# Kernel optimization log

Hardware: AMD Instinct MI355X
Metric: run time of the kernel (lower is better)

Reference implementation:

```python
import jax, jax.numpy as jnp
import numpy as np

B, T, C = 2, 2048, 2048
NH, NKV = 16, 4
HD = C // NH  # 128
DFF = 4 * C


def rmsnorm(x):
    eps = jnp.finfo(x.dtype).eps
    return x * jax.lax.rsqrt(jnp.mean(jnp.square(x), axis=-1, keepdims=True) + eps)


def rotary(x, cos, sin):
    # x: [B,T,H,HD], cos/sin: [1,T,1,HD//2]
    d = x.shape[-1] // 2
    x1, x2 = x[..., :d], x[..., d:]
    return jnp.concatenate([x1 * cos + x2 * sin, -x1 * sin + x2 * cos], axis=-1)


def setup_inputs() -> dict:
    key = jax.random.key(0)
    ks = jax.random.split(key, 8)
    x = jax.random.normal(ks[0], (B, T, C), jnp.float32)
    inv_freq = 1.0 / (10000.0 ** (jnp.arange(HD // 2, dtype=jnp.float32) / (HD // 2)))
    ang = jnp.arange(T, dtype=jnp.float32)[:, None] * inv_freq[None, :]  # [T, HD//2]
    cos = jnp.cos(ang)[None, :, None, :]
    sin = jnp.sin(ang)[None, :, None, :]
    s = 0.02
    wq = jax.random.normal(ks[1], (C, NH * HD), jnp.float32) * s
    wk = jax.random.normal(ks[2], (C, NKV * HD), jnp.float32) * s
    wv = jax.random.normal(ks[3], (C, NKV * HD), jnp.float32) * s
    wo = jax.random.normal(ks[4], (C, C), jnp.float32) * s
    w_fc = jax.random.normal(ks[5], (C, DFF), jnp.float32) * s
    w_proj = jax.random.normal(ks[6], (DFF, C), jnp.float32) * s
    return {"x": x, "cos": cos, "sin": sin, "wq": wq, "wk": wk, "wv": wv,
            "wo": wo, "w_fc": w_fc, "w_proj": w_proj}


def reference(x, cos, sin, wq, wk, wv, wo, w_fc, w_proj):
    # --- attention sublayer (pre-norm residual) ---
    h = rmsnorm(x)
    q = (h @ wq).reshape(B, T, NH, HD)
    k = (h @ wk).reshape(B, T, NKV, HD)
    v = (h @ wv).reshape(B, T, NKV, HD)
    q = rmsnorm(rotary(q, cos, sin))
    k = rmsnorm(rotary(k, cos, sin))
    rep = NH // NKV
    k = jnp.repeat(k, rep, axis=2)  # [B,T,NH,HD]
    v = jnp.repeat(v, rep, axis=2)
    scale = 1.0 / np.sqrt(HD)
    scores = jnp.einsum('bqhd,bkhd->bhqk', q, k) * scale
    causal = jnp.tril(jnp.ones((T, T), dtype=bool))
    scores = jnp.where(causal[None, None], scores, jnp.finfo(scores.dtype).min)
    attn = jax.nn.softmax(scores, axis=-1)
    y = jnp.einsum('bhqk,bkhd->bqhd', attn, v).reshape(B, T, C)
    x = x + y @ wo
    # --- MLP sublayer (relu^2) ---
    h = rmsnorm(x)
    h = jnp.square(jax.nn.relu(h @ w_fc))
    x = x + h @ w_proj
    return x
```

## Files before the change

kernel.cpp:

```cpp
#include <hip/hip_runtime.h>
#include <cstdint>
#include <cstddef>


#define B_    2
#define T_    2048
#define C_    2048
#define NH_   16
#define NKV_  4
#define HD_   128
#define DFF_  8192
#define EPS_  1.1920928955078125e-07f

typedef short          bf16x8 __attribute__((ext_vector_type(8)));
typedef float          f32x4  __attribute__((ext_vector_type(4)));
typedef unsigned short u16;
typedef unsigned short u16x8  __attribute__((ext_vector_type(8)));
typedef unsigned short u16x4  __attribute__((ext_vector_type(4)));

__device__ __forceinline__ u16 f2bf(float f) {
    unsigned u = __float_as_uint(f);
    unsigned r = u + 0x7fffu + ((u >> 16) & 1u);
    return (u16)(r >> 16);
}
__device__ __forceinline__ float bf2f(u16 u) {
    return __uint_as_float((unsigned)u << 16);
}

__device__ __forceinline__ void load_lds16(const void* g, void* l) {
    __builtin_amdgcn_global_load_lds(
        (__attribute__((address_space(1))) void*)(g),
        (__attribute__((address_space(3))) void*)(l), 16, 0, 0);
}

__device__ __forceinline__ unsigned lds_addr(const void* p) {
    return (unsigned)(unsigned long long)(__attribute__((address_space(3))) const void*)p;
}

struct TD  { const float* src; u16* dst; int K, N, boff; };
struct TD6 { TD t[6]; };

#define TRBLKS_ 10752

__global__ void prep_all(TD6 d, const float* __restrict__ x, u16* __restrict__ hout) {
    __shared__ u16 tile[32][136];
    __shared__ float part[4];
    int bid = blockIdx.x;
    int tid = threadIdx.x;

    if (bid >= TRBLKS_) {
        int row = bid - TRBLKS_;
        const float4* xr = (const float4*)(x + (size_t)row * C_);
        float4 a = xr[tid];
        float4 b = xr[tid + 256];
        float ss = a.x * a.x + a.y * a.y + a.z * a.z + a.w * a.w
                 + b.x * b.x + b.y * b.y + b.z * b.z + b.w * b.w;
        for (int m = 1; m < 64; m <<= 1) ss += __shfl_xor(ss, m, 64);
        if ((tid & 63) == 0) part[tid >> 6] = ss;
        __syncthreads();
        float tot = part[0] + part[1] + part[2] + part[3];
        float sc = rsqrtf(tot * (1.0f / C_) + EPS_);
        u16x4 o1, o2;
        o1[0] = f2bf(a.x * sc); o1[1] = f2bf(a.y * sc); o1[2] = f2bf(a.z * sc); o1[3] = f2bf(a.w * sc);
        o2[0] = f2bf(b.x * sc); o2[1] = f2bf(b.y * sc); o2[2] = f2bf(b.z * sc); o2[3] = f2bf(b.w * sc);
        u16x4* orow = (u16x4*)(hout + (size_t)row * C_);
        orow[tid]       = o1;
        orow[tid + 256] = o2;
        return;
    }

    int di = 0;
    for (int i = 5; i > 0; --i) if (bid >= d.t[i].boff) { di = i; break; }
    const float* src = d.t[di].src;
    u16* dst = d.t[di].dst;
    int K = d.t[di].K, N = d.t[di].N;
    int lb = bid - d.t[di].boff;
    int nx = N >> 5;
    int n0 = (lb % nx) * 32;
    int k0 = (lb / nx) * 128;

    int kr = tid >> 3;
    int nc = (tid & 7) * 4;
    for (int r = 0; r < 4; ++r) {
        int kk = kr + r * 32;
        float4 v = *(const float4*)&src[(size_t)(k0 + kk) * N + n0 + nc];
        tile[nc + 0][kk] = f2bf(v.x);
        tile[nc + 1][kk] = f2bf(v.y);
        tile[nc + 2][kk] = f2bf(v.z);
        tile[nc + 3][kk] = f2bf(v.w);
    }
    __syncthreads();
    int nL = tid >> 4;
    int kc = (tid & 15) * 8;
    for (int w2 = 0; w2 < 2; ++w2) {
        int n = nL + w2 * 16;
        u16x8 o = *(const u16x8*)&tile[n][kc];
        *(u16x8*)&dst[(size_t)(n0 + n) * K + k0 + kc] = o;
    }
}

__global__ void transpose_v(const u16* __restrict__ vb, u16* __restrict__ Vt) {
    int bx   = blockIdx.x;
    int dblk = bx & 1;
    int t0   = (bx >> 1) * 32;
    int kvh  = blockIdx.y, b = blockIdx.z;
    int dl   = threadIdx.x & 63;
    int tc   = threadIdx.x >> 6;
    int d    = dblk * 64 + dl;
    u16x8 v8;
    for (int j = 0; j < 8; ++j) {
        int t = t0 + tc * 8 + j;
        v8[j] = vb[((size_t)(b * T_ + t) * NKV_ + kvh) * HD_ + d];
    }
    *(u16x8*)(Vt + ((size_t)((b * NKV_ + kvh) * HD_ + d)) * T_ + t0 + tc * 8) = v8;
}

__global__ void reduce_rms(const float* __restrict__ x, const u16* __restrict__ p0,
                           const u16* __restrict__ p1, float* __restrict__ x2,
                           u16* __restrict__ hout) {
    int row = blockIdx.x;
    const float4* xr = (const float4*)(x + (size_t)row * C_);
    const u16x4* a0 = (const u16x4*)(p0 + (size_t)row * C_);
    const u16x4* a1 = (const u16x4*)(p1 + (size_t)row * C_);
    float4 v[2];
    float ss = 0.f;
    for (int h = 0; h < 2; ++h) {
        int idx = threadIdx.x + h * 256;
        float4 xv = xr[idx];
        u16x4 b0 = a0[idx], b1 = a1[idx];
        v[h].x = xv.x + bf2f(b0[0]) + bf2f(b1[0]);
        v[h].y = xv.y + bf2f(b0[1]) + bf2f(b1[1]);
        v[h].z = xv.z + bf2f(b0[2]) + bf2f(b1[2]);
        v[h].w = xv.w + bf2f(b0[3]) + bf2f(b1[3]);
        ss += v[h].x * v[h].x + v[h].y * v[h].y + v[h].z * v[h].z + v[h].w * v[h].w;
    }
    for (int m = 1; m < 64; m <<= 1) ss += __shfl_xor(ss, m, 64);
    __shared__ float part[4];
    if ((threadIdx.x & 63) == 0) part[threadIdx.x >> 6] = ss;
    __syncthreads();
    float tot = part[0] + part[1] + part[2] + part[3];
    float sc = rsqrtf(tot * (1.0f / C_) + EPS_);
    float4* x2r = (float4*)(x2 + (size_t)row * C_);
    u16x4* hr   = (u16x4*)(hout + (size_t)row * C_);
    for (int h = 0; h < 2; ++h) {
        int idx = threadIdx.x + h * 256;
        x2r[idx] = v[h];
        u16x4 o;
        o[0] = f2bf(v[h].x * sc); o[1] = f2bf(v[h].y * sc);
        o[2] = f2bf(v[h].z * sc); o[3] = f2bf(v[h].w * sc);
        hr[idx] = o;
    }
}

__global__ void reduce_out(const float* __restrict__ x2, const u16* __restrict__ p0,
                           const u16* __restrict__ p1, float* __restrict__ out) {
    size_t i = (size_t)blockIdx.x * 256 + threadIdx.x;
    float4 xv = ((const float4*)x2)[i];
    u16x4 b0 = ((const u16x4*)p0)[i];
    u16x4 b1 = ((const u16x4*)p1)[i];
    float4 o;
    o.x = xv.x + bf2f(b0[0]) + bf2f(b1[0]);
    o.y = xv.y + bf2f(b0[1]) + bf2f(b1[1]);
    o.z = xv.z + bf2f(b0[2]) + bf2f(b1[2]);
    o.w = xv.w + bf2f(b0[3]) + bf2f(b1[3]);
    ((float4*)out)[i] = o;
}

__global__ void rope_rms2(const float* __restrict__ Xq, const float* __restrict__ Xk,
                          const float* __restrict__ cosb, const float* __restrict__ sinb,
                          u16* __restrict__ Oq, u16* __restrict__ Ok) {
    int gw   = (int)((blockIdx.x * blockDim.x + threadIdx.x) >> 6);
    int lane = threadIdx.x & 63;
    const float* X; u16* O; int t;
    if (gw < B_ * T_ * NH_) {
        X = Xq + (size_t)gw * HD_;  O = Oq + (size_t)gw * HD_;  t = (gw / NH_) % T_;
    } else {
        int w2 = gw - B_ * T_ * NH_;
        X = Xk + (size_t)w2 * HD_;  O = Ok + (size_t)w2 * HD_;  t = (w2 / NKV_) % T_;
    }
    float x1 = X[lane];
    float x2 = X[64 + lane];
    float c  = cosb[t * 64 + lane];
    float sn = sinb[t * 64 + lane];
    float r1 = x1 * c + x2 * sn;
    float r2 = x2 * c - x1 * sn;
    float ss = r1 * r1 + r2 * r2;
    for (int m = 1; m < 64; m <<= 1) ss += __shfl_xor(ss, m, 64);
    float sc = rsqrtf(ss * (1.0f / HD_) + EPS_);
    O[lane]      = f2bf(r1 * sc);
    O[64 + lane] = f2bf(r2 * sc);
}


#define BARRIER() do { __builtin_amdgcn_s_barrier();                     \
                       asm volatile("" ::: "memory"); } while (0)
#define LGKMN(N)  do { asm volatile("s_waitcnt lgkmcnt(" #N ")" ::: "memory");\
                       __builtin_amdgcn_sched_barrier(0); } while (0)

#define DSR(dst, base, lit)                                              \
    asm volatile("ds_read_b128 %0, %1 offset:" lit : "=v"(dst) : "v"(base))

#define READ_AFL() do {                                                  \
    DSR(afl[0][0], aB0, "0");     DSR(afl[0][1], aB1, "0");              \
    DSR(afl[1][0], aB0, "2048");  DSR(afl[1][1], aB1, "2048");           \
    DSR(afl[2][0], aB0, "4096");  DSR(afl[2][1], aB1, "4096");           \
    DSR(afl[3][0], aB0, "6144");  DSR(afl[3][1], aB1, "6144"); } while (0)

#define READ_AFH() do {                                                  \
    DSR(afh[0][0], aB0, "8192");  DSR(afh[0][1], aB1, "8192");           \
    DSR(afh[1][0], aB0, "10240"); DSR(afh[1][1], aB1, "10240");          \
    DSR(afh[2][0], aB0, "12288"); DSR(afh[2][1], aB1, "12288");          \
    DSR(afh[3][0], aB0, "14336"); DSR(afh[3][1], aB1, "14336"); } while (0)

#define READ_BL() do {                                                   \
    DSR(bl[0][0], bB0, "0");     DSR(bl[0][1], bB1, "0");                \
    DSR(bl[1][0], bB0, "2048");  DSR(bl[1][1], bB1, "2048"); } while (0)

#define READ_BH() do {                                                   \
    DSR(bh[0][0], bB0, "4096");  DSR(bh[0][1], bB1, "4096");             \
    DSR(bh[1][0], bB0, "6144");  DSR(bh[1][1], bB1, "6144"); } while (0)

#define MFMA_BLK(AF, BF, MB, NB)                                             \
    _Pragma("unroll")                                                        \
    for (int ks = 0; ks < 2; ++ks)                                           \
        _Pragma("unroll")                                                    \
        for (int mi = 0; mi < 4; ++mi)                                       \
            _Pragma("unroll")                                                \
            for (int ni = 0; ni < 2; ++ni)                                   \
                acc[MB + mi][NB + ni] =                                      \
                    __builtin_amdgcn_mfma_f32_16x16x32_bf16(                 \
                        AF[mi][ks], BF[ni][ks], acc[MB + mi][NB + ni], 0, 0, 0);

template <int EPI>
__launch_bounds__(512, 1)
__global__ void gemm256(const u16* __restrict__ A, const u16* __restrict__ Bt,
                        void* __restrict__ out, void* __restrict__ out2,
                        void* __restrict__ out3, int M, int N, int K, int Ks) {
    __shared__ __attribute__((aligned(16))) u16 sh[65536];

    int tid  = threadIdx.x;
    int l    = tid & 63;
    int w    = tid >> 6;
    int l16  = l & 15;
    int quad = l >> 4;
    int sw   = l & 7;
    int wm   = w >> 2, wn = w & 3;

    int nwg = gridDim.x * gridDim.y;
    int id  = blockIdx.y * gridDim.x + blockIdx.x;
    int sid = (id & 7) * (nwg >> 3) + (id >> 3);
    int bn  = sid % gridDim.x;
    int bm  = sid / gridDim.x;

    size_t koff = (size_t)blockIdx.z * K;
    int nt = K >> 6;

    int csrc = ((l & 7) ^ ((l >> 3) & 7)) * 8;
    int srow = w * 8 + (l >> 3);
    const u16* Ast = A  + (size_t)(bm * 256 + srow) * Ks + koff + csrc;
    const u16* Bst = Bt + (size_t)(bn * 256 + srow) * Ks + koff + csrc;

    auto stageA = [&](int h, int kk, int buf) {
        const u16* g = Ast + (size_t)(h * 128) * Ks + kk;
        u16* d = sh + buf * 32768 + h * 8192 + w * 512;
        load_lds16(g, d);
        load_lds16(g + (size_t)64 * Ks, d + 4096);
    };
    auto stageB = [&](int h, int kk, int buf) {
        const u16* g = Bst + (size_t)(h * 128) * Ks + kk;
        u16* d = sh + buf * 32768 + (2 + h) * 8192 + w * 512;
        load_lds16(g, d);
        load_lds16(g + (size_t)64 * Ks, d + 4096);
    };

    f32x4 acc[8][4];
#pragma unroll
    for (int m = 0; m < 8; ++m)
#pragma unroll
        for (int n = 0; n < 4; ++n) acc[m][n] = (f32x4){0.f, 0.f, 0.f, 0.f};

    stageB(0, 0, 0); stageA(0, 0, 0); stageA(1, 0, 0); stageB(1, 0, 0);
    stageB(0, 64, 1); stageA(0, 64, 1);
    asm volatile("s_waitcnt vmcnt(4)" ::: "memory");
    BARRIER();

    bf16x8 afl[4][2], afh[4][2], bl[2][2], bh[2][2];
    unsigned shbase = lds_addr(sh);
    unsigned ck0 = (unsigned)((quad ^ sw) * 16);
    unsigned ck1 = ck0 ^ 64u;
    unsigned Aoff = (unsigned)(wm * 16384 + l16 * 128);
    unsigned Boff = (unsigned)((2 + (wn >> 1)) * 16384 + (wn & 1) * 8192
                               + l16 * 128);
    unsigned aB0c = shbase + Aoff + ck0, aB1c = shbase + Aoff + ck1;
    unsigned bB0c = shbase + Boff + ck0, bB1c = shbase + Boff + ck1;

    for (int t = 0; t < nt; ++t) {
        int buf = t & 1;
        unsigned bo  = (unsigned)buf << 16;
        unsigned aB0 = aB0c + bo, aB1 = aB1c + bo;
        unsigned bB0 = bB0c + bo, bB1 = bB1c + bo;
        bool s1 = (t + 1 < nt), s2 = (t + 2 < nt);

        READ_AFL();
        READ_BL();
        READ_BH();
        READ_AFH();
        if (s1) { stageA(1, (t + 1) * 64, buf ^ 1);
                  stageB(1, (t + 1) * 64, buf ^ 1); }

        LGKMN(12);
        __builtin_amdgcn_s_setprio(1);
        MFMA_BLK(afl, bl, 0, 0);
        __builtin_amdgcn_s_setprio(0);

        LGKMN(8);
        __builtin_amdgcn_s_setprio(1);
        MFMA_BLK(afl, bh, 0, 2);
        __builtin_amdgcn_s_setprio(0);

        LGKMN(0);
        BARRIER();
        if (s2) { stageB(0, (t + 2) * 64, buf);
                  stageA(0, (t + 2) * 64, buf); }

        __builtin_amdgcn_s_setprio(1);
        MFMA_BLK(afh, bl, 4, 0);
        MFMA_BLK(afh, bh, 4, 2);
        __builtin_amdgcn_s_setprio(0);

        if (s2)      asm volatile("s_waitcnt vmcnt(4)" ::: "memory");
        else if (s1) asm volatile("s_waitcnt vmcnt(0)" ::: "memory");
        BARRIER();
    }

#pragma unroll
    for (int m = 0; m < 8; ++m)
#pragma unroll
        for (int n = 0; n < 4; ++n)
#pragma unroll
            for (int r = 0; r < 4; ++r) {
                int rg = bm * 256 + wm * 128 + m * 16 + quad * 4 + r;
                int cg = bn * 256 + wn * 64 + n * 16 + l16;
                float v = acc[m][n][r];
                if (EPI == 2) {
                    float tv = fmaxf(v, 0.f);
                    ((u16*)out)[(size_t)rg * N + cg] = f2bf(tv * tv);
                } else if (EPI == 4) {
                    if (cg < 2048)      ((float*)out)[(size_t)rg * 2048 + cg] = v;
                    else if (cg < 2560) ((float*)out2)[(size_t)rg * 512 + (cg - 2048)] = v;
                    else                ((u16*)out3)[(size_t)rg * 512 + (cg - 2560)] = f2bf(v);
                } else {
                    u16* p = (blockIdx.z == 0) ? (u16*)out : (u16*)out2;
                    p[(size_t)rg * N + cg] = f2bf(v);
                }
            }
}

__launch_bounds__(256, 2)
__global__ void flash_attn2(const u16* __restrict__ Q, const u16* __restrict__ Kb,
                            const u16* __restrict__ Vt, u16* __restrict__ Y) {
    __shared__ __attribute__((aligned(16))) u16 Qs[128 * 128];
    __shared__ __attribute__((aligned(16))) u16 Ks[64 * 128];
    __shared__ __attribute__((aligned(16))) u16 Vs[2][128 * 64];

    int bid = blockIdx.x;
    int half = bid >> 8, idx = bid & 255;
    int qr = idx & 15;
    int qt = half ? (15 - qr) : qr;
    int bh = (idx >> 4) | (half << 4);
    int b = bh >> 4, h = bh & 15;
    int kvh = h >> 2;
    int q0 = qt * 128;

    int tid = threadIdx.x, lane = tid & 63, wave = tid >> 6;
    int quad = lane >> 4, l16 = lane & 15;

    {
        int r = lane >> 4;
        for (int c = 0; c < 8; ++c) {
            int row = wave * 32 + c * 4 + r;
            int cc = ((lane & 15) ^ (row & 15)) * 8;
            const u16* g = Q + ((size_t)((b * T_ + q0 + row) * NH_ + h)) * HD_ + cc;
            load_lds16(g, &Qs[(wave * 32 + c * 4) * 128]);
        }
    }
    __syncthreads();

    bf16x8 qf[2][4];
    for (int qtile = 0; qtile < 2; ++qtile)
        for (int kd = 0; kd < 4; ++kd)
            qf[qtile][kd] = *(const bf16x8*)&Qs[(wave * 32 + qtile * 16 + l16) * 128
                                               + (((kd * 4 + quad) ^ l16) * 8)];
    u16* Ps = &Qs[wave * 32 * 128];

    auto stageK = [&](int kt) {
        int r = lane >> 4;
        for (int c = 0; c < 4; ++c) {
            int row = wave * 16 + c * 4 + r;
            int cc = ((lane & 15) ^ (row & 15)) * 8;
            const u16* g = Kb + ((size_t)((b * T_ + kt * 64 + row) * NKV_ + kvh)) * HD_ + cc;
            load_lds16(g, &Ks[(wave * 16 + c * 4) * 128]);
        }
    };
    auto stageV = [&](int kt, int vb) {
        int dr = lane >> 3;
        int kc = (((lane & 7) ^ dr)) * 8;
        for (int c = 0; c < 4; ++c) {
            int drow = wave * 32 + c * 8 + dr;
            const u16* g = Vt + ((size_t)((b * NKV_ + kvh) * HD_ + drow)) * T_ + kt * 64 + kc;
            load_lds16(g, &Vs[vb][(wave * 32 + c * 8) * 64]);
        }
    };

    f32x4 zero = {0.f, 0.f, 0.f, 0.f};
    f32x4 o[2][8];
    for (int qtile = 0; qtile < 2; ++qtile)
        for (int dt = 0; dt < 8; ++dt) o[qtile][dt] = zero;
    float m_i[2] = {-__builtin_inff(), -__builtin_inff()};
    float l_i[2] = {0.f, 0.f};
    const float s2s = 0.08838834764831845f * 1.4426950408889634f;

    int nkt = 2 * qt + 2;
    stageK(0); stageV(0, 0);

    for (int kt = 0; kt < nkt; ++kt) {
        int vcur = kt & 1;
        __syncthreads();

        f32x4 st[2][4];
        for (int qtile = 0; qtile < 2; ++qtile)
            for (int tn = 0; tn < 4; ++tn) st[qtile][tn] = zero;
        __builtin_amdgcn_s_setprio(1);
        for (int tn = 0; tn < 4; ++tn)
            for (int kd = 0; kd < 4; ++kd) {
                bf16x8 kf = *(const bf16x8*)&Ks[(tn * 16 + l16) * 128
                                                + (((kd * 4 + quad) ^ l16) * 8)];
                st[0][tn] = __builtin_amdgcn_mfma_f32_16x16x32_bf16(kf, qf[0][kd], st[0][tn], 0, 0, 0);
                st[1][tn] = __builtin_amdgcn_mfma_f32_16x16x32_bf16(kf, qf[1][kd], st[1][tn], 0, 0, 0);
            }
        __builtin_amdgcn_s_setprio(0);

        __syncthreads();
        if (kt + 1 < nkt) {
            stageK(kt + 1);
            stageV(kt + 1, vcur ^ 1);
        }

        for (int qtile = 0; qtile < 2; ++qtile) {
            int qmin = q0 + wave * 32 + qtile * 16;
            int qg   = qmin + l16;
            bool need_mask = (kt * 64 + 63 > qmin);
            float mx = -__builtin_inff();
            for (int tn = 0; tn < 4; ++tn)
                for (int r = 0; r < 4; ++r) {
                    float v = st[qtile][tn][r] * s2s;
                    if (need_mask) {
                        int key = kt * 64 + tn * 16 + quad * 4 + r;
                        if (key > qg) v = -__builtin_inff();
                    }
                    st[qtile][tn][r] = v;
                    mx = fmaxf(mx, v);
                }
            mx = fmaxf(mx, __shfl_xor(mx, 16, 64));
            mx = fmaxf(mx, __shfl_xor(mx, 32, 64));
            float mnew = fmaxf(m_i[qtile], mx);
            float al   = exp2f(m_i[qtile] - mnew);
            m_i[qtile] = mnew;
            float sum = 0.f;
            for (int tn = 0; tn < 4; ++tn) {
                u16x4 pk;
                for (int r = 0; r < 4; ++r) {
                    float e = exp2f(st[qtile][tn][r] - mnew);
                    sum += e;
                    pk[r] = f2bf(e);
                }
                *(u16x4*)&Ps[(qtile * 16 + l16) * 72 + tn * 16 + quad * 4] = pk;
            }
            sum += __shfl_xor(sum, 16, 64);
            sum += __shfl_xor(sum, 32, 64);
            l_i[qtile] = l_i[qtile] * al + sum;
            float aB[4];
            for (int r = 0; r < 4; ++r) aB[r] = __shfl(al, quad * 4 + r, 64);
            for (int dt = 0; dt < 8; ++dt)
                for (int r = 0; r < 4; ++r) o[qtile][dt][r] *= aB[r];
        }

        bf16x8 pf[2][2];
        for (int qtile = 0; qtile < 2; ++qtile)
            for (int ks = 0; ks < 2; ++ks)
                pf[qtile][ks] = *(const bf16x8*)&Ps[(qtile * 16 + l16) * 72 + ks * 32 + quad * 8];
        __builtin_amdgcn_s_setprio(1);
        for (int ks = 0; ks < 2; ++ks)
            for (int dt = 0; dt < 8; ++dt) {
                bf16x8 vf = *(const bf16x8*)&Vs[vcur][(dt * 16 + l16) * 64
                                                + (((ks * 4 + quad) ^ (l16 & 7)) * 8)];
                o[0][dt] = __builtin_amdgcn_mfma_f32_16x16x32_bf16(pf[0][ks], vf, o[0][dt], 0, 0, 0);
                o[1][dt] = __builtin_amdgcn_mfma_f32_16x16x32_bf16(pf[1][ks], vf, o[1][dt], 0, 0, 0);
            }
        __builtin_amdgcn_s_setprio(0);
    }

    for (int qtile = 0; qtile < 2; ++qtile) {
        float inv = 1.0f / l_i[qtile];
        float iB[4];
        for (int r = 0; r < 4; ++r) iB[r] = __shfl(inv, quad * 4 + r, 64);
        for (int r = 0; r < 4; ++r) {
            int qg = q0 + wave * 32 + qtile * 16 + quad * 4 + r;
            u16* yr = Y + ((size_t)((b * T_ + qg) * NH_ + h)) * HD_;
            for (int dt = 0; dt < 8; ++dt)
                yr[dt * 16 + l16] = f2bf(o[qtile][dt][r] * iB[r]);
        }
    }
}

extern "C" void kernel_launch(void* const* d_in, const int* in_sizes, int n_in,
                              void* d_out, int out_size, void* d_ws, size_t ws_size,
                              hipStream_t stream) {
    const float* x     = (const float*)d_in[0];
    const float* cosb  = (const float*)d_in[1];
    const float* sinb  = (const float*)d_in[2];
    const float* wq    = (const float*)d_in[3];
    const float* wk    = (const float*)d_in[4];
    const float* wv    = (const float*)d_in[5];
    const float* wo    = (const float*)d_in[6];
    const float* wfc   = (const float*)d_in[7];
    const float* wproj = (const float*)d_in[8];

    char* ws = (char*)d_ws;
    size_t off = 0;
    auto alloc = [&](size_t bytes) { char* p = ws + off; off += (bytes + 255) & ~(size_t)255; return p; };

    u16*   wqkvT  = (u16*)alloc((size_t)3072 * C_ * 2);
    u16*   woT    = (u16*)alloc((size_t)C_ * C_ * 2);
    u16*   wfcT   = (u16*)alloc((size_t)DFF_ * C_ * 2);
    u16*   wprojT = (u16*)alloc((size_t)C_ * DFF_ * 2);
    u16*   hbuf   = (u16*)alloc((size_t)B_ * T_ * C_ * 2);
    float* x2     = (float*)alloc((size_t)B_ * T_ * C_ * 4);
    u16*   ybuf   = (u16*)alloc((size_t)B_ * T_ * C_ * 2);
    u16*   Vtb    = (u16*)alloc((size_t)B_ * NKV_ * HD_ * T_ * 2);
    char*  scratch = alloc((size_t)B_ * T_ * DFF_ * 2);
    float* q_tmp  = (float*)scratch;
    float* k_tmp  = (float*)(scratch + (size_t)B_ * T_ * C_ * 4);
    u16*   qb     = (u16*)(scratch + (size_t)B_ * T_ * C_ * 4 + (size_t)B_ * T_ * 512 * 4);
    u16*   kb     = (u16*)((char*)qb + (size_t)B_ * T_ * C_ * 2);
    u16*   vb     = (u16*)((char*)kb + (size_t)B_ * T_ * 512 * 2);
    u16*   wop1   = (u16*)scratch;
    u16*   ffbuf  = (u16*)scratch;

    const int M = B_ * T_;
    dim3 tb(256);

    TD6 td;
    td.t[0] = { wq,    wqkvT,                       C_,   C_,   0 };
    td.t[1] = { wk,    wqkvT + (size_t)2048 * C_,   C_,   512,  1024 };
    td.t[2] = { wv,    wqkvT + (size_t)2560 * C_,   C_,   512,  1280 };
    td.t[3] = { wo,    woT,                         C_,   C_,   1536 };
    td.t[4] = { wfc,   wfcT,                        C_,   DFF_, 2560 };
    td.t[5] = { wproj, wprojT,                      DFF_, C_,   6656 };
    prep_all<<<dim3(TRBLKS_ + M), tb, 0, stream>>>(td, x, hbuf);

    gemm256<4><<<dim3(3072 / 256, M / 256), dim3(512), 0, stream>>>(
        hbuf, wqkvT, q_tmp, k_tmp, vb, M, 3072, C_, C_);

    rope_rms2<<<dim3((B_ * T_ * (NH_ + NKV_)) / 4), tb, 0, stream>>>(q_tmp, k_tmp, cosb, sinb, qb, kb);
    transpose_v<<<dim3(128, NKV_, B_), tb, 0, stream>>>(vb, Vtb);

    flash_attn2<<<dim3(512), tb, 0, stream>>>(qb, kb, Vtb, ybuf);

    gemm256<5><<<dim3(C_ / 256, M / 256, 2), dim3(512), 0, stream>>>(
        ybuf, woT, hbuf, wop1, nullptr, M, C_, C_ / 2, C_);

    reduce_rms<<<M, tb, 0, stream>>>(x, hbuf, wop1, x2, hbuf);

    gemm256<2><<<dim3(DFF_ / 256, M / 256), dim3(512), 0, stream>>>(
        hbuf, wfcT, ffbuf, nullptr, nullptr, M, DFF_, C_, C_);

    gemm256<5><<<dim3(C_ / 256, M / 256, 2), dim3(512), 0, stream>>>(
        ffbuf, wprojT, hbuf, ybuf, nullptr, M, C_, DFF_ / 2, DFF_);

    reduce_out<<<dim3((M * C_) / 1024), tb, 0, stream>>>(x2, hbuf, ybuf, (float*)d_out);
}
```

Measured before the change: 685.1 us.

## Merge rope and V-transpose launches; regroup GEMM tile-to-block mapping

Folds the V transpose kernel into the rope/rmsnorm kernel as extra leading blocks, saving one launch and its tail gap. It also changes the GEMM workgroup swizzle so each XCD-strided chunk walks column groups of 4 or 8 N-tiles down M, aiming for better L2 reuse of weight tiles. The new mapping relies on grid dimensions dividing evenly into the group sizes.

```diff
diff --git a/kernel.cpp b/kernel.cpp
--- a/kernel.cpp
+++ b/kernel.cpp
@@ -99,20 +99,50 @@
     }
 }
 
-__global__ void transpose_v(const u16* __restrict__ vb, u16* __restrict__ Vt) {
-    int bx   = blockIdx.x;
-    int dblk = bx & 1;
-    int t0   = (bx >> 1) * 32;
-    int kvh  = blockIdx.y, b = blockIdx.z;
-    int dl   = threadIdx.x & 63;
-    int tc   = threadIdx.x >> 6;
-    int d    = dblk * 64 + dl;
-    u16x8 v8;
-    for (int j = 0; j < 8; ++j) {
-        int t = t0 + tc * 8 + j;
-        v8[j] = vb[((size_t)(b * T_ + t) * NKV_ + kvh) * HD_ + d];
-    }
-    *(u16x8*)(Vt + ((size_t)((b * NKV_ + kvh) * HD_ + d)) * T_ + t0 + tc * 8) = v8;
+#define TVB_ 1024
+
+__global__ void rope_tv(const float* __restrict__ Xq, const float* __restrict__ Xk,
+                        const float* __restrict__ cosb, const float* __restrict__ sinb,
+                        u16* __restrict__ Oq, u16* __restrict__ Ok,
+                        const u16* __restrict__ vb, u16* __restrict__ Vt) {
+    int bid = blockIdx.x;
+    if (bid < TVB_) {
+        int bxx  = bid & 127;
+        int kvh  = (bid >> 7) & 3;
+        int b    = bid >> 9;
+        int dblk = bxx & 1;
+        int t0   = (bxx >> 1) * 32;
+        int dl   = threadIdx.x & 63;
+        int tc   = threadIdx.x >> 6;
+        int d    = dblk * 64 + dl;
+        u16x8 v8;
+        for (int j = 0; j < 8; ++j) {
+            int t = t0 + tc * 8 + j;
+            v8[j] = vb[((size_t)(b * T_ + t) * NKV_ + kvh) * HD_ + d];
+        }
+        *(u16x8*)(Vt + ((size_t)((b * NKV_ + kvh) * HD_ + d)) * T_ + t0 + tc * 8) = v8;
+        return;
+    }
+    int gw   = (int)(((bid - TVB_) * blockDim.x + threadIdx.x) >> 6);
+    int lane = threadIdx.x & 63;
+    const float* X; u16* O; int t;
+    if (gw < B_ * T_ * NH_) {
+        X = Xq + (size_t)gw * HD_;  O = Oq + (size_t)gw * HD_;  t = (gw / NH_) % T_;
+    } else {
+        int w2 = gw - B_ * T_ * NH_;
+        X = Xk + (size_t)w2 * HD_;  O = Ok + (size_t)w2 * HD_;  t = (w2 / NKV_) % T_;
+    }
+    float x1 = X[lane];
+    float x2 = X[64 + lane];
+    float c  = cosb[t * 64 + lane];
+    float sn = sinb[t * 64 + lane];
+    float r1 = x1 * c + x2 * sn;
+    float r2 = x2 * c - x1 * sn;
+    float ss = r1 * r1 + r2 * r2;
+    for (int m = 1; m < 64; m <<= 1) ss += __shfl_xor(ss, m, 64);
+    float sc = rsqrtf(ss * (1.0f / HD_) + EPS_);
+    O[lane]      = f2bf(r1 * sc);
+    O[64 + lane] = f2bf(r2 * sc);
 }
 
 __global__ void reduce_rms(const float* __restrict__ x, const u16* __restrict__ p0,
@@ -166,31 +196,6 @@
     ((float4*)out)[i] = o;
 }
 
-__global__ void rope_rms2(const float* __restrict__ Xq, const float* __restrict__ Xk,
-                          const float* __restrict__ cosb, const float* __restrict__ sinb,
-                          u16* __restrict__ Oq, u16* __restrict__ Ok) {
-    int gw   = (int)((blockIdx.x * blockDim.x + threadIdx.x) >> 6);
-    int lane = threadIdx.x & 63;
-    const float* X; u16* O; int t;
-    if (gw < B_ * T_ * NH_) {
-        X = Xq + (size_t)gw * HD_;  O = Oq + (size_t)gw * HD_;  t = (gw / NH_) % T_;
-    } else {
-        int w2 = gw - B_ * T_ * NH_;
-        X = Xk + (size_t)w2 * HD_;  O = Ok + (size_t)w2 * HD_;  t = (w2 / NKV_) % T_;
-    }
-    float x1 = X[lane];
-    float x2 = X[64 + lane];
-    float c  = cosb[t * 64 + lane];
-    float sn = sinb[t * 64 + lane];
-    float r1 = x1 * c + x2 * sn;
-    float r2 = x2 * c - x1 * sn;
-    float ss = r1 * r1 + r2 * r2;
-    for (int m = 1; m < 64; m <<= 1) ss += __shfl_xor(ss, m, 64);
-    float sc = rsqrtf(ss * (1.0f / HD_) + EPS_);
-    O[lane]      = f2bf(r1 * sc);
-    O[64 + lane] = f2bf(r2 * sc);
-}
-
 
 #define BARRIER() do { __builtin_amdgcn_s_barrier();                     \
                        asm volatile("" ::: "memory"); } while (0)
@@ -248,9 +253,14 @@
 
     int nwg = gridDim.x * gridDim.y;
     int id  = blockIdx.y * gridDim.x + blockIdx.x;
-    int sid = (id & 7) * (nwg >> 3) + (id >> 3);
-    int bn  = sid % gridDim.x;
-    int bm  = sid / gridDim.x;
+    int cpx = nwg >> 3;
+    int sid = (id & 7) * cpx + (id >> 3);
+    int GN   = (cpx >= 64) ? 8 : 4;
+    int span = gridDim.y * GN;
+    int bnb  = sid / span;
+    int r0   = sid % span;
+    int bm   = r0 / GN;
+    int bn   = bnb * GN + (r0 % GN);
 
     size_t koff = (size_t)blockIdx.z * K;
     int nt = K >> 6;
@@ -562,8 +572,8 @@
     gemm256<4><<<dim3(3072 / 256, M / 256), dim3(512), 0, stream>>>(
         hbuf, wqkvT, q_tmp, k_tmp, vb, M, 3072, C_, C_);
 
-    rope_rms2<<<dim3((B_ * T_ * (NH_ + NKV_)) / 4), tb, 0, stream>>>(q_tmp, k_tmp, cosb, sinb, qb, kb);
-    transpose_v<<<dim3(128, NKV_, B_), tb, 0, stream>>>(vb, Vtb);
+    rope_tv<<<dim3(TVB_ + (B_ * T_ * (NH_ + NKV_)) / 4), tb, 0, stream>>>(
+        q_tmp, k_tmp, cosb, sinb, qb, kb, vb, Vtb);
 
     flash_attn2<<<dim3(512), tb, 0, stream>>>(qb, kb, Vtb, ybuf);
 
```

Result: no change. 694.2 us (+1.3%).
